# Kernel optimization log

Hardware: AMD Instinct MI355X
Metric: run time of the kernel (lower is better)

Reference implementation:

```python
import jax, jax.numpy as jnp
import numpy as np

B, S, H = 2, 2048, 2048
NH, G = 16, 4
HD = H // NH          # 128
REP = NH // G         # 4 query heads per KV group
KV = G * HD           # 512


def setup_inputs() -> dict:
    key = jax.random.key(0)
    ks = jax.random.split(key, 10)
    s = 0.02
    X = jax.random.normal(ks[0], (B, S, H), dtype=jnp.float32)
    Wq = jax.random.normal(ks[1], (H, H), dtype=jnp.float32) * s
    bq = jnp.zeros((H,), dtype=jnp.float32)
    Wk = jax.random.normal(ks[2], (H, KV), dtype=jnp.float32) * s
    bk = jnp.zeros((KV,), dtype=jnp.float32)
    Wv = jax.random.normal(ks[3], (H, KV), dtype=jnp.float32) * s
    bv = jnp.zeros((KV,), dtype=jnp.float32)
    Wo = jax.random.normal(ks[4], (H, H), dtype=jnp.float32) * s
    bo = jnp.zeros((H,), dtype=jnp.float32)
    # causal mask: 1 where attention is disallowed (strict upper triangle)
    casual_mask = jnp.triu(jnp.ones((S, S), dtype=jnp.float32), k=1)[None, None]
    return {"X": X, "Wq": Wq, "bq": bq, "Wk": Wk, "bk": bk,
            "Wv": Wv, "bv": bv, "Wo": Wo, "bo": bo,
            "casual_mask": casual_mask}


def reference(X, Wq, bq, Wk, bk, Wv, bv, Wo, bo, casual_mask):
    # projections
    q = X @ Wq + bq                          # [B,S,H]
    k = X @ Wk + bk                          # [B,S,G*HD]
    v = X @ Wv + bv                          # [B,S,G*HD]
    # split heads; q grouped as (group, rep) to match torch expand ordering
    q = q.reshape(B, S, NH, HD).transpose(0, 2, 1, 3)       # [B,NH,S,HD]
    q = q.reshape(B, G, REP, S, HD)                          # [B,G,REP,S,HD]
    k = k.reshape(B, S, G, HD).transpose(0, 2, 1, 3)         # [B,G,S,HD]
    v = v.reshape(B, S, G, HD).transpose(0, 2, 1, 3)         # [B,G,S,HD]
    scale = 1.0 / jnp.sqrt(jnp.float32(HD))
    scores = jnp.einsum('bgrqd,bgkd->bgrqk', q, k) * scale   # [B,G,REP,S,S]
    scores = scores + casual_mask * (-1e9)
    probs = jax.nn.softmax(scores, axis=-1)
    out = jnp.einsum('bgrqk,bgkd->bgrqd', probs, v)          # [B,G,REP,S,HD]
    out = out.reshape(B, NH, S, HD).transpose(0, 2, 1, 3).reshape(B, S, H)
    return out @ Wo + bo
```

## Files before the change

kernel.cpp:

```cpp
#include <hip/hip_runtime.h>

#define B_   2
#define S_   2048
#define H_   2048
#define NH_  16
#define G_   4
#define HD_  128
#define KV_  512
#define HQKV 3072

typedef __attribute__((ext_vector_type(8))) short bf16x8;
typedef __attribute__((ext_vector_type(4))) float f32x4;

__device__ __forceinline__ unsigned short f2bf(float f) {
    unsigned u = __float_as_uint(f);
    u += 0x7fff + ((u >> 16) & 1);
    return (unsigned short)(u >> 16);
}
__device__ __forceinline__ float bf2f(unsigned short s) {
    return __uint_as_float(((unsigned)s) << 16);
}

#define GLDS16(gsrc, ldst)                                                            \
    __builtin_amdgcn_global_load_lds(                                                 \
        (const __attribute__((address_space(1))) void*)(gsrc),                        \
        (__attribute__((address_space(3))) void*)(ldst), 16, 0, 0)

__global__ void k_cvt_bf16(const float* __restrict__ in, unsigned short* __restrict__ out, int n4) {
    int i = blockIdx.x * blockDim.x + threadIdx.x;
    if (i >= n4) return;
    float4 v = ((const float4*)in)[i];
    ushort4 o;
    o.x = f2bf(v.x); o.y = f2bf(v.y); o.z = f2bf(v.z); o.w = f2bf(v.w);
    ((ushort4*)out)[i] = o;
}

__global__ void k_transpose_cvt(const float* __restrict__ in, unsigned short* __restrict__ out,
                                int R, int C) {
    __shared__ float t[32][33];
    int c0 = blockIdx.x * 32, r0 = blockIdx.y * 32;
    int tx = threadIdx.x, ty = threadIdx.y;
#pragma unroll
    for (int i = 0; i < 4; ++i)
        t[ty + i*8][tx] = in[(size_t)(r0 + ty + i*8) * C + c0 + tx];
    __syncthreads();
#pragma unroll
    for (int i = 0; i < 4; ++i)
        out[(size_t)(c0 + ty + i*8) * R + r0 + tx] = f2bf(t[tx][ty + i*8]);
}

__global__ void k_concat_bias(const float* __restrict__ bq, const float* __restrict__ bk,
                              const float* __restrict__ bv, float* __restrict__ out) {
    int i = blockIdx.x * 256 + threadIdx.x;
    if (i >= HQKV) return;
    out[i] = (i < H_) ? bq[i] : (i < H_ + KV_ ? bk[i - H_] : bv[i - H_ - KV_]);
}

__global__ void k_transpose_v(const unsigned short* __restrict__ in, unsigned short* __restrict__ out) {
    __shared__ unsigned short t[32][33];
    int b = blockIdx.z;
    int c0 = blockIdx.x * 32, s0 = blockIdx.y * 32;
    int tx = threadIdx.x, ty = threadIdx.y;
#pragma unroll
    for (int i = 0; i < 4; ++i)
        t[ty + i*8][tx] = in[((size_t)b * S_ + s0 + ty + i*8) * HQKV + (H_ + KV_) + c0 + tx];
    __syncthreads();
#pragma unroll
    for (int i = 0; i < 4; ++i)
        out[((size_t)b * KV_ + c0 + ty + i*8) * S_ + s0 + tx] = t[tx][ty + i*8];
}

template <bool BF16OUT>
__global__ __launch_bounds__(256) void k_gemm_bt(
    const unsigned short* __restrict__ A, const unsigned short* __restrict__ Bt,
    const float* __restrict__ bias, void* __restrict__ Cout, int M, int N, int K) {
    __shared__ __align__(16) unsigned short As[128 * 64];
    __shared__ __align__(16) unsigned short Bs[128 * 64];
    const int tid = threadIdx.x, lane = tid & 63, w = tid >> 6;
    const int l15 = lane & 15, l4 = lane >> 4;
    const int wr = w >> 1, wc = w & 1;
    const int m0 = blockIdx.x * 128, n0 = blockIdx.y * 128;
    f32x4 acc[4][4] = {};

    for (int kt = 0; kt < K; kt += 64) {
        __syncthreads();
#pragma unroll
        for (int i = 0; i < 4; ++i) {
            int p = (w * 4 + i) * 64 + lane;
            int row = p >> 3, c = (p & 7) ^ (row & 7);
            GLDS16(A + (size_t)(m0 + row) * K + kt + c * 8, As + (size_t)(w * 4 + i) * 512);
        }
#pragma unroll
        for (int i = 0; i < 4; ++i) {
            int p = (w * 4 + i) * 64 + lane;
            int row = p >> 3, c = (p & 7) ^ (row & 7);
            GLDS16(Bt + (size_t)(n0 + row) * K + kt + c * 8, Bs + (size_t)(w * 4 + i) * 512);
        }
        __syncthreads();
#pragma unroll
        for (int ks = 0; ks < 2; ++ks) {
            bf16x8 af[4], bfr[4];
#pragma unroll
            for (int m = 0; m < 4; ++m) {
                int row = wr * 64 + m * 16 + l15;
                int ch = (ks * 4 + l4) ^ (row & 7);
                af[m] = *(const bf16x8*)(As + row * 64 + ch * 8);
            }
#pragma unroll
            for (int n = 0; n < 4; ++n) {
                int row = wc * 64 + n * 16 + l15;
                int ch = (ks * 4 + l4) ^ (row & 7);
                bfr[n] = *(const bf16x8*)(Bs + row * 64 + ch * 8);
            }
#pragma unroll
            for (int m = 0; m < 4; ++m)
#pragma unroll
                for (int n = 0; n < 4; ++n)
                    acc[m][n] = __builtin_amdgcn_mfma_f32_16x16x32_bf16(af[m], bfr[n], acc[m][n], 0, 0, 0);
        }
    }
#pragma unroll
    for (int m = 0; m < 4; ++m) {
        int row = m0 + wr * 64 + m * 16 + l4 * 4;
#pragma unroll
        for (int n = 0; n < 4; ++n) {
            int col = n0 + wc * 64 + n * 16 + l15;
            float bv = bias[col];
#pragma unroll
            for (int r = 0; r < 4; ++r) {
                float v = acc[m][n][r] + bv;
                if (BF16OUT)
                    ((unsigned short*)Cout)[(size_t)(row + r) * N + col] = f2bf(v);
                else
                    ((float*)Cout)[(size_t)(row + r) * N + col] = v;
            }
        }
    }
}

__global__ __launch_bounds__(256) void k_flash(
    const unsigned short* __restrict__ QKV,
    const unsigned short* __restrict__ VT,
    unsigned short* __restrict__ Oa) {
    __shared__ __align__(16) unsigned short Ks[2][64 * 128];
    __shared__ __align__(16) unsigned short Vs[2][128 * 64];
    __shared__ __align__(16) unsigned short Ps[4][16][68];
    const int tid = threadIdx.x, lane = tid & 63, w = tid >> 6;
    const int l15 = lane & 15, l4 = lane >> 4;
    const int bid = blockIdx.x;
    const int xcd = bid & 7, idx = bid >> 3;
    const int bh = xcd * 4 + (idx & 3);
    const int pr = idx >> 2;
    const int b = bh >> 4, nh = bh & 15, g = nh >> 2;
    const float sc2 = 0.08838834764831843f * 1.4426950408889634f;

    const unsigned short* kgbase = QKV + (size_t)b * S_ * HQKV + H_ + g * HD_;
    const unsigned short* vgbase = VT + ((size_t)b * KV_ + g * HD_) * S_;

    for (int half = 0; half < 2; ++half) {
        const int qt = half ? (31 - pr) : pr;
        const int q0 = qt * 64;
        const int qbase = q0 + w * 16;

        bf16x8 qf[4];
#pragma unroll
        for (int kb = 0; kb < 4; ++kb) {
            bf16x8 raw = *(const bf16x8*)(QKV + (size_t)(b * S_ + qbase + l15) * HQKV +
                                          nh * HD_ + kb * 32 + l4 * 8);
            bf16x8 sq;
#pragma unroll
            for (int e = 0; e < 8; ++e)
                sq[e] = (short)f2bf(bf2f((unsigned short)raw[e]) * sc2);
            qf[kb] = sq;
        }

        f32x4 o[8] = {};
        float mrow[4], lrow[4];
#pragma unroll
        for (int r = 0; r < 4; ++r) { mrow[r] = -1e30f; lrow[r] = 0.f; }

        auto issue = [&](int kt, int cb) {
            const int kv0 = kt * 64;
#pragma unroll
            for (int i = 0; i < 4; ++i) {
                int p = i * 256 + tid;
                int row = p >> 4, c = (p & 15) ^ (row & 15);
                GLDS16(kgbase + (size_t)(kv0 + row) * HQKV + c * 8,
                       &Ks[cb][(i * 256 + w * 64) * 8]);
            }
#pragma unroll
            for (int i = 0; i < 4; ++i) {
                int p = i * 256 + tid;
                int row = p >> 3, c = (p & 7) ^ (row & 7);
                GLDS16(vgbase + (size_t)row * S_ + kv0 + c * 8,
                       &Vs[cb][(i * 256 + w * 64) * 8]);
            }
        };

        auto compute = [&](int cb, int kt) {
            const int kv0 = kt * 64;
            f32x4 s[4] = {};
#pragma unroll
            for (int kb = 0; kb < 4; ++kb) {
                bf16x8 kf[4];
#pragma unroll
                for (int n = 0; n < 4; ++n) {
                    int row = n * 16 + l15;
                    int sl = (kb * 4 + l4) ^ (row & 15);
                    kf[n] = *(const bf16x8*)(&Ks[cb][(row * 16 + sl) * 8]);
                }
#pragma unroll
                for (int n = 0; n < 4; ++n)
                    s[n] = __builtin_amdgcn_mfma_f32_16x16x32_bf16(qf[kb], kf[n], s[n], 0, 0, 0);
            }
            if (kv0 + 63 > qbase) {
#pragma unroll
                for (int n = 0; n < 4; ++n)
#pragma unroll
                    for (int r = 0; r < 4; ++r) {
                        int kcol = kv0 + n * 16 + l15;
                        int qrow = qbase + l4 * 4 + r;
                        if (kcol > qrow) s[n][r] = -1e30f;
                    }
            }
            float vm[4];
#pragma unroll
            for (int r = 0; r < 4; ++r) {
                float v = fmaxf(fmaxf(s[0][r], s[1][r]), fmaxf(s[2][r], s[3][r]));
                v = fmaxf(v, __shfl_xor(v, 1));
                v = fmaxf(v, __shfl_xor(v, 2));
                v = fmaxf(v, __shfl_xor(v, 4));
                v = fmaxf(v, __shfl_xor(v, 8));
                vm[r] = v;
            }
            int needs = 0;
#pragma unroll
            for (int r = 0; r < 4; ++r) needs |= (vm[r] > mrow[r] + 8.0f) ? 1 : 0;
            if (__any(needs)) {
                float sf[4];
#pragma unroll
                for (int r = 0; r < 4; ++r) {
                    float mn = fmaxf(mrow[r], vm[r]);
                    sf[r] = exp2f(mrow[r] - mn);
                    mrow[r] = mn;
                    lrow[r] *= sf[r];
                }
#pragma unroll
                for (int nc = 0; nc < 8; ++nc) {
                    f32x4 t = o[nc];
                    t[0] *= sf[0]; t[1] *= sf[1]; t[2] *= sf[2]; t[3] *= sf[3];
                    o[nc] = t;
                }
            }
            float rs[4] = {0.f, 0.f, 0.f, 0.f};
#pragma unroll
            for (int n = 0; n < 4; ++n)
#pragma unroll
                for (int r = 0; r < 4; ++r) {
                    float p = exp2f(s[n][r] - mrow[r]);
                    s[n][r] = p;
                    rs[r] += p;
                }
#pragma unroll
            for (int r = 0; r < 4; ++r) {
                float t = rs[r];
                t += __shfl_xor(t, 1); t += __shfl_xor(t, 2);
                t += __shfl_xor(t, 4); t += __shfl_xor(t, 8);
                lrow[r] += t;
            }
#pragma unroll
            for (int n = 0; n < 4; ++n)
#pragma unroll
                for (int r = 0; r < 4; ++r)
                    Ps[w][l4 * 4 + r][n * 16 + l15] = f2bf(s[n][r]);
#pragma unroll
            for (int kb = 0; kb < 2; ++kb) {
                bf16x8 pf = *(const bf16x8*)(&Ps[w][l15][kb * 32 + l4 * 8]);
#pragma unroll
                for (int nc = 0; nc < 8; ++nc) {
                    int row = nc * 16 + l15;
                    int sl = (kb * 4 + l4) ^ (row & 7);
                    bf16x8 vf = *(const bf16x8*)(&Vs[cb][(row * 8 + sl) * 8]);
                    o[nc] = __builtin_amdgcn_mfma_f32_16x16x32_bf16(pf, vf, o[nc], 0, 0, 0);
                }
            }
        };

        const int nkt = qt + 1;
        __syncthreads();
        issue(0, 0);
        asm volatile("s_waitcnt vmcnt(0)" ::: "memory");
        __builtin_amdgcn_s_barrier();
        __builtin_amdgcn_sched_barrier(0);

        for (int kt = 0; kt < nkt; ++kt) {
            const int cb = kt & 1;
            if (kt + 1 < nkt) issue(kt + 1, cb ^ 1);
            compute(cb, kt);
            asm volatile("s_waitcnt vmcnt(0) lgkmcnt(0)" ::: "memory");
            __builtin_amdgcn_s_barrier();
            __builtin_amdgcn_sched_barrier(0);
        }

#pragma unroll
        for (int r = 0; r < 4; ++r) {
            float inv = 1.0f / lrow[r];
            int qrow = qbase + l4 * 4 + r;
            size_t base = (size_t)(b * S_ + qrow) * H_ + nh * HD_;
#pragma unroll
            for (int nc = 0; nc < 8; ++nc)
                Oa[base + nc * 16 + l15] = f2bf(o[nc][r] * inv);
        }
    }
}

extern "C" void kernel_launch(void* const* d_in, const int* in_sizes, int n_in,
                              void* d_out, int out_size, void* d_ws, size_t ws_size,
                              hipStream_t stream) {
    const float* X  = (const float*)d_in[0];
    const float* Wq = (const float*)d_in[1];
    const float* bq = (const float*)d_in[2];
    const float* Wk = (const float*)d_in[3];
    const float* bk = (const float*)d_in[4];
    const float* Wv = (const float*)d_in[5];
    const float* bv = (const float*)d_in[6];
    const float* Wo = (const float*)d_in[7];
    const float* bo = (const float*)d_in[8];
    float* out = (float*)d_out;

    if (ws_size < 67200000) return;
    char* ws = (char*)d_ws;
    unsigned short* Xb   = (unsigned short*)(ws);
    unsigned short* WqkvT= (unsigned short*)(ws + 16777216);
    unsigned short* WoT  = (unsigned short*)(ws + 29360128);
    unsigned short* QKV  = (unsigned short*)(ws + 37748736);
    unsigned short* VbT  = (unsigned short*)(ws + 62914560);
    float*          bqkv = (float*)(ws + 67108864);
    unsigned short* AOb  = Xb;

    k_cvt_bf16<<<(B_ * S_ * H_ / 4 + 255) / 256, 256, 0, stream>>>(X, Xb, B_ * S_ * H_ / 4);
    k_transpose_cvt<<<dim3(H_ / 32, H_ / 32), dim3(32, 8), 0, stream>>>(Wq, WqkvT, H_, H_);
    k_transpose_cvt<<<dim3(KV_ / 32, H_ / 32), dim3(32, 8), 0, stream>>>(Wk, WqkvT + (size_t)H_ * H_, H_, KV_);
    k_transpose_cvt<<<dim3(KV_ / 32, H_ / 32), dim3(32, 8), 0, stream>>>(Wv, WqkvT + (size_t)(H_ + KV_) * H_, H_, KV_);
    k_transpose_cvt<<<dim3(H_ / 32, H_ / 32), dim3(32, 8), 0, stream>>>(Wo, WoT, H_, H_);
    k_concat_bias<<<(HQKV + 255) / 256, 256, 0, stream>>>(bq, bk, bv, bqkv);

    k_gemm_bt<true><<<dim3(32, 24), 256, 0, stream>>>(Xb, WqkvT, bqkv, QKV, 4096, HQKV, 2048);

    k_transpose_v<<<dim3(KV_ / 32, S_ / 32, B_), dim3(32, 8), 0, stream>>>(QKV, VbT);
    k_flash<<<dim3(512), 256, 0, stream>>>(QKV, VbT, AOb);

    k_gemm_bt<false><<<dim3(32, 16), 256, 0, stream>>>(AOb, WoT, bo, out, 4096, 2048, 2048);
}
```

Measured before the change: 240.3 us.

## Read K/V fragments directly from global memory in flash kernel, fold Q scale into GEMM

The flash-attention kernel drops its double-buffered LDS staging of K and V tiles and the per-tile barriers. Each wave now loads its MFMA K and V fragments straight from global memory, relying on L2/L1 caching because the four waves share the same tiles. Removing the LDS buffers lets the kernel declare a higher occupancy target (launch_bounds 256,4). The softmax scale on Q moves into the QKV GEMM epilogue so the flash kernel loads Q directly. The trade is that shared tiles are no longer reused through LDS, so each wave issues redundant global loads with uncoalesced strided rows, in exchange for no synchronization and more resident waves.

After: 425.4 us. 1.77x slower.

```diff
diff --git a/kernel.cpp b/kernel.cpp
--- a/kernel.cpp
+++ b/kernel.cpp
@@ -17,14 +17,13 @@
     u += 0x7fff + ((u >> 16) & 1);
     return (unsigned short)(u >> 16);
 }
-__device__ __forceinline__ float bf2f(unsigned short s) {
-    return __uint_as_float(((unsigned)s) << 16);
-}
 
 #define GLDS16(gsrc, ldst)                                                            \
     __builtin_amdgcn_global_load_lds(                                                 \
         (const __attribute__((address_space(1))) void*)(gsrc),                        \
         (__attribute__((address_space(3))) void*)(ldst), 16, 0, 0)
+
+#define SC2F (0.08838834764831843f * 1.4426950408889634f)
 
 __global__ void k_cvt_bf16(const float* __restrict__ in, unsigned short* __restrict__ out, int n4) {
     int i = blockIdx.x * blockDim.x + threadIdx.x;
@@ -70,7 +69,7 @@
         out[((size_t)b * KV_ + c0 + ty + i*8) * S_ + s0 + tx] = t[tx][ty + i*8];
 }
 
-template <bool BF16OUT>
+template <bool BF16OUT, bool QSCALE>
 __global__ __launch_bounds__(256) void k_gemm_bt(
     const unsigned short* __restrict__ A, const unsigned short* __restrict__ Bt,
     const float* __restrict__ bias, void* __restrict__ Cout, int M, int N, int K) {
@@ -129,6 +128,7 @@
 #pragma unroll
             for (int r = 0; r < 4; ++r) {
                 float v = acc[m][n][r] + bv;
+                if (QSCALE) { if (col < H_) v *= SC2F; }
                 if (BF16OUT)
                     ((unsigned short*)Cout)[(size_t)(row + r) * N + col] = f2bf(v);
                 else
@@ -138,12 +138,10 @@
     }
 }
 
-__global__ __launch_bounds__(256) void k_flash(
+__global__ __launch_bounds__(256, 4) void k_flash(
     const unsigned short* __restrict__ QKV,
     const unsigned short* __restrict__ VT,
     unsigned short* __restrict__ Oa) {
-    __shared__ __align__(16) unsigned short Ks[2][64 * 128];
-    __shared__ __align__(16) unsigned short Vs[2][128 * 64];
     __shared__ __align__(16) unsigned short Ps[4][16][68];
     const int tid = threadIdx.x, lane = tid & 63, w = tid >> 6;
     const int l15 = lane & 15, l4 = lane >> 4;
@@ -152,7 +150,6 @@
     const int bh = xcd * 4 + (idx & 3);
     const int pr = idx >> 2;
     const int b = bh >> 4, nh = bh & 15, g = nh >> 2;
-    const float sc2 = 0.08838834764831843f * 1.4426950408889634f;
 
     const unsigned short* kgbase = QKV + (size_t)b * S_ * HQKV + H_ + g * HD_;
     const unsigned short* vgbase = VT + ((size_t)b * KV_ + g * HD_) * S_;
@@ -164,51 +161,28 @@
 
         bf16x8 qf[4];
 #pragma unroll
-        for (int kb = 0; kb < 4; ++kb) {
-            bf16x8 raw = *(const bf16x8*)(QKV + (size_t)(b * S_ + qbase + l15) * HQKV +
-                                          nh * HD_ + kb * 32 + l4 * 8);
-            bf16x8 sq;
-#pragma unroll
-            for (int e = 0; e < 8; ++e)
-                sq[e] = (short)f2bf(bf2f((unsigned short)raw[e]) * sc2);
-            qf[kb] = sq;
-        }
+        for (int kb = 0; kb < 4; ++kb)
+            qf[kb] = *(const bf16x8*)(QKV + (size_t)(b * S_ + qbase + l15) * HQKV +
+                                      nh * HD_ + kb * 32 + l4 * 8);
 
         f32x4 o[8] = {};
         float mrow[4], lrow[4];
 #pragma unroll
         for (int r = 0; r < 4; ++r) { mrow[r] = -1e30f; lrow[r] = 0.f; }
 
-        auto issue = [&](int kt, int cb) {
+        const int nkt = qt + 1;
+        for (int kt = 0; kt < nkt; ++kt) {
             const int kv0 = kt * 64;
-#pragma unroll
-            for (int i = 0; i < 4; ++i) {
-                int p = i * 256 + tid;
-                int row = p >> 4, c = (p & 15) ^ (row & 15);
-                GLDS16(kgbase + (size_t)(kv0 + row) * HQKV + c * 8,
-                       &Ks[cb][(i * 256 + w * 64) * 8]);
-            }
-#pragma unroll
-            for (int i = 0; i < 4; ++i) {
-                int p = i * 256 + tid;
-                int row = p >> 3, c = (p & 7) ^ (row & 7);
-                GLDS16(vgbase + (size_t)row * S_ + kv0 + c * 8,
-                       &Vs[cb][(i * 256 + w * 64) * 8]);
-            }
-        };
-
-        auto compute = [&](int cb, int kt) {
-            const int kv0 = kt * 64;
+            const unsigned short* kti = kgbase + (size_t)kv0 * HQKV;
+            const unsigned short* vti = vgbase + kv0;
+
             f32x4 s[4] = {};
 #pragma unroll
             for (int kb = 0; kb < 4; ++kb) {
                 bf16x8 kf[4];
 #pragma unroll
-                for (int n = 0; n < 4; ++n) {
-                    int row = n * 16 + l15;
-                    int sl = (kb * 4 + l4) ^ (row & 15);
-                    kf[n] = *(const bf16x8*)(&Ks[cb][(row * 16 + sl) * 8]);
-                }
+                for (int n = 0; n < 4; ++n)
+                    kf[n] = *(const bf16x8*)(kti + (size_t)(n * 16 + l15) * HQKV + kb * 32 + l4 * 8);
 #pragma unroll
                 for (int n = 0; n < 4; ++n)
                     s[n] = __builtin_amdgcn_mfma_f32_16x16x32_bf16(qf[kb], kf[n], s[n], 0, 0, 0);
@@ -278,30 +252,11 @@
                 bf16x8 pf = *(const bf16x8*)(&Ps[w][l15][kb * 32 + l4 * 8]);
 #pragma unroll
                 for (int nc = 0; nc < 8; ++nc) {
-                    int row = nc * 16 + l15;
-                    int sl = (kb * 4 + l4) ^ (row & 7);
-                    bf16x8 vf = *(const bf16x8*)(&Vs[cb][(row * 8 + sl) * 8]);
+                    bf16x8 vf = *(const bf16x8*)(vti + (size_t)(nc * 16 + l15) * S_ + kb * 32 + l4 * 8);
                     o[nc] = __builtin_amdgcn_mfma_f32_16x16x32_bf16(pf, vf, o[nc], 0, 0, 0);
                 }
             }
-        };
-
-        const int nkt = qt + 1;
-        __syncthreads();
-        issue(0, 0);
-        asm volatile("s_waitcnt vmcnt(0)" ::: "memory");
-        __builtin_amdgcn_s_barrier();
-        __builtin_amdgcn_sched_barrier(0);
-
-        for (int kt = 0; kt < nkt; ++kt) {
-            const int cb = kt & 1;
-            if (kt + 1 < nkt) issue(kt + 1, cb ^ 1);
-            compute(cb, kt);
-            asm volatile("s_waitcnt vmcnt(0) lgkmcnt(0)" ::: "memory");
-            __builtin_amdgcn_s_barrier();
-            __builtin_amdgcn_sched_barrier(0);
-        }
-
+        }
 #pragma unroll
         for (int r = 0; r < 4; ++r) {
             float inv = 1.0f / lrow[r];
@@ -345,10 +300,10 @@
     k_transpose_cvt<<<dim3(H_ / 32, H_ / 32), dim3(32, 8), 0, stream>>>(Wo, WoT, H_, H_);
     k_concat_bias<<<(HQKV + 255) / 256, 256, 0, stream>>>(bq, bk, bv, bqkv);
 
-    k_gemm_bt<true><<<dim3(32, 24), 256, 0, stream>>>(Xb, WqkvT, bqkv, QKV, 4096, HQKV, 2048);
+    k_gemm_bt<true, true><<<dim3(32, 24), 256, 0, stream>>>(Xb, WqkvT, bqkv, QKV, 4096, HQKV, 2048);
 
     k_transpose_v<<<dim3(KV_ / 32, S_ / 32, B_), dim3(32, 8), 0, stream>>>(QKV, VbT);
     k_flash<<<dim3(512), 256, 0, stream>>>(QKV, VbT, AOb);
 
-    k_gemm_bt<false><<<dim3(32, 16), 256, 0, stream>>>(AOb, WoT, bo, out, 4096, 2048, 2048);
-}
+    k_gemm_bt<false, false><<<dim3(32, 16), 256, 0, stream>>>(AOb, WoT, bo, out, 4096, 2048, 2048);
+}
```

## Split long causal query tiles across two blocks and merge with a combine kernel

Applied to the files above, without the earlier changes.

The flash kernel stops pairing short and long query tiles in one block. It now launches 1536 blocks: tiles 0-15 are done whole, and tiles 16-31 are split into KV ranges [0,16) and [16,qt]. Each split writes an unnormalized partial with its m/l statistics, and a new combine kernel merges them. It also folds the Q softmax scale into the QKV GEMM epilogue, single-buffers K with a mid-iteration reload, shrinks the P staging buffer, and sets launch_bounds occupancy 3. The aim is more parallelism and better load balance, at the cost of an extra kernel, partial-output traffic, and bf16 rounding of unnormalized partials.

Result: slower. 250.8 us (+4.4%).

```diff
diff --git a/kernel.cpp b/kernel.cpp
--- a/kernel.cpp
+++ b/kernel.cpp
@@ -26,6 +26,8 @@
         (const __attribute__((address_space(1))) void*)(gsrc),                        \
         (__attribute__((address_space(3))) void*)(ldst), 16, 0, 0)
 
+#define SC2F (0.08838834764831843f * 1.4426950408889634f)
+
 __global__ void k_cvt_bf16(const float* __restrict__ in, unsigned short* __restrict__ out, int n4) {
     int i = blockIdx.x * blockDim.x + threadIdx.x;
     if (i >= n4) return;
@@ -70,7 +72,7 @@
         out[((size_t)b * KV_ + c0 + ty + i*8) * S_ + s0 + tx] = t[tx][ty + i*8];
 }
 
-template <bool BF16OUT>
+template <bool BF16OUT, bool QSCALE>
 __global__ __launch_bounds__(256) void k_gemm_bt(
     const unsigned short* __restrict__ A, const unsigned short* __restrict__ Bt,
     const float* __restrict__ bias, void* __restrict__ Cout, int M, int N, int K) {
@@ -129,6 +131,7 @@
 #pragma unroll
             for (int r = 0; r < 4; ++r) {
                 float v = acc[m][n][r] + bv;
+                if (QSCALE) { if (col < H_) v *= SC2F; }
                 if (BF16OUT)
                     ((unsigned short*)Cout)[(size_t)(row + r) * N + col] = f2bf(v);
                 else
@@ -138,170 +141,170 @@
     }
 }
 
-__global__ __launch_bounds__(256) void k_flash(
+__global__ __launch_bounds__(256, 3) void k_flash(
     const unsigned short* __restrict__ QKV,
     const unsigned short* __restrict__ VT,
-    unsigned short* __restrict__ Oa) {
-    __shared__ __align__(16) unsigned short Ks[2][64 * 128];
+    unsigned short* __restrict__ Oa,
+    unsigned short* __restrict__ part1,
+    float* __restrict__ mlbuf) {
+    __shared__ __align__(16) unsigned short Ks[64 * 128];
     __shared__ __align__(16) unsigned short Vs[2][128 * 64];
-    __shared__ __align__(16) unsigned short Ps[4][16][68];
+    __shared__ __align__(16) unsigned short Ps[4][16][40];
     const int tid = threadIdx.x, lane = tid & 63, w = tid >> 6;
     const int l15 = lane & 15, l4 = lane >> 4;
     const int bid = blockIdx.x;
     const int xcd = bid & 7, idx = bid >> 3;
     const int bh = xcd * 4 + (idx & 3);
-    const int pr = idx >> 2;
+    const int jidx = idx >> 2;
     const int b = bh >> 4, nh = bh & 15, g = nh >> 2;
-    const float sc2 = 0.08838834764831843f * 1.4426950408889634f;
+
+    int qt, t0, t1, mode;
+    if (jidx < 16) { qt = 16 + jidx; t0 = 0; t1 = 16; mode = 1; }
+    else {
+        int k = jidx - 16, j = k >> 1;
+        if ((k & 1) == 0) { qt = 31 - j; t0 = 16; t1 = qt + 1; mode = 2; }
+        else              { qt = 15 - j; t0 = 0;  t1 = qt + 1; mode = 0; }
+    }
+    const int qbase = qt * 64 + w * 16;
 
     const unsigned short* kgbase = QKV + (size_t)b * S_ * HQKV + H_ + g * HD_;
     const unsigned short* vgbase = VT + ((size_t)b * KV_ + g * HD_) * S_;
 
-    for (int half = 0; half < 2; ++half) {
-        const int qt = half ? (31 - pr) : pr;
-        const int q0 = qt * 64;
-        const int qbase = q0 + w * 16;
-
-        bf16x8 qf[4];
-#pragma unroll
-        for (int kb = 0; kb < 4; ++kb) {
-            bf16x8 raw = *(const bf16x8*)(QKV + (size_t)(b * S_ + qbase + l15) * HQKV +
-                                          nh * HD_ + kb * 32 + l4 * 8);
-            bf16x8 sq;
-#pragma unroll
-            for (int e = 0; e < 8; ++e)
-                sq[e] = (short)f2bf(bf2f((unsigned short)raw[e]) * sc2);
-            qf[kb] = sq;
-        }
-
-        f32x4 o[8] = {};
-        float mrow[4], lrow[4];
-#pragma unroll
-        for (int r = 0; r < 4; ++r) { mrow[r] = -1e30f; lrow[r] = 0.f; }
-
-        auto issue = [&](int kt, int cb) {
-            const int kv0 = kt * 64;
-#pragma unroll
-            for (int i = 0; i < 4; ++i) {
-                int p = i * 256 + tid;
-                int row = p >> 4, c = (p & 15) ^ (row & 15);
-                GLDS16(kgbase + (size_t)(kv0 + row) * HQKV + c * 8,
-                       &Ks[cb][(i * 256 + w * 64) * 8]);
-            }
-#pragma unroll
-            for (int i = 0; i < 4; ++i) {
-                int p = i * 256 + tid;
-                int row = p >> 3, c = (p & 7) ^ (row & 7);
-                GLDS16(vgbase + (size_t)row * S_ + kv0 + c * 8,
-                       &Vs[cb][(i * 256 + w * 64) * 8]);
-            }
-        };
-
-        auto compute = [&](int cb, int kt) {
-            const int kv0 = kt * 64;
-            f32x4 s[4] = {};
-#pragma unroll
-            for (int kb = 0; kb < 4; ++kb) {
-                bf16x8 kf[4];
-#pragma unroll
-                for (int n = 0; n < 4; ++n) {
-                    int row = n * 16 + l15;
-                    int sl = (kb * 4 + l4) ^ (row & 15);
-                    kf[n] = *(const bf16x8*)(&Ks[cb][(row * 16 + sl) * 8]);
-                }
-#pragma unroll
-                for (int n = 0; n < 4; ++n)
-                    s[n] = __builtin_amdgcn_mfma_f32_16x16x32_bf16(qf[kb], kf[n], s[n], 0, 0, 0);
-            }
-            if (kv0 + 63 > qbase) {
-#pragma unroll
-                for (int n = 0; n < 4; ++n)
-#pragma unroll
-                    for (int r = 0; r < 4; ++r) {
-                        int kcol = kv0 + n * 16 + l15;
-                        int qrow = qbase + l4 * 4 + r;
-                        if (kcol > qrow) s[n][r] = -1e30f;
-                    }
-            }
-            float vm[4];
-#pragma unroll
-            for (int r = 0; r < 4; ++r) {
-                float v = fmaxf(fmaxf(s[0][r], s[1][r]), fmaxf(s[2][r], s[3][r]));
-                v = fmaxf(v, __shfl_xor(v, 1));
-                v = fmaxf(v, __shfl_xor(v, 2));
-                v = fmaxf(v, __shfl_xor(v, 4));
-                v = fmaxf(v, __shfl_xor(v, 8));
-                vm[r] = v;
-            }
-            int needs = 0;
-#pragma unroll
-            for (int r = 0; r < 4; ++r) needs |= (vm[r] > mrow[r] + 8.0f) ? 1 : 0;
-            if (__any(needs)) {
-                float sf[4];
-#pragma unroll
-                for (int r = 0; r < 4; ++r) {
-                    float mn = fmaxf(mrow[r], vm[r]);
-                    sf[r] = exp2f(mrow[r] - mn);
-                    mrow[r] = mn;
-                    lrow[r] *= sf[r];
-                }
-#pragma unroll
-                for (int nc = 0; nc < 8; ++nc) {
-                    f32x4 t = o[nc];
-                    t[0] *= sf[0]; t[1] *= sf[1]; t[2] *= sf[2]; t[3] *= sf[3];
-                    o[nc] = t;
-                }
-            }
-            float rs[4] = {0.f, 0.f, 0.f, 0.f};
-#pragma unroll
-            for (int n = 0; n < 4; ++n)
-#pragma unroll
-                for (int r = 0; r < 4; ++r) {
-                    float p = exp2f(s[n][r] - mrow[r]);
-                    s[n][r] = p;
-                    rs[r] += p;
-                }
-#pragma unroll
-            for (int r = 0; r < 4; ++r) {
-                float t = rs[r];
-                t += __shfl_xor(t, 1); t += __shfl_xor(t, 2);
-                t += __shfl_xor(t, 4); t += __shfl_xor(t, 8);
-                lrow[r] += t;
-            }
-#pragma unroll
-            for (int n = 0; n < 4; ++n)
-#pragma unroll
-                for (int r = 0; r < 4; ++r)
-                    Ps[w][l4 * 4 + r][n * 16 + l15] = f2bf(s[n][r]);
-#pragma unroll
-            for (int kb = 0; kb < 2; ++kb) {
-                bf16x8 pf = *(const bf16x8*)(&Ps[w][l15][kb * 32 + l4 * 8]);
-#pragma unroll
-                for (int nc = 0; nc < 8; ++nc) {
-                    int row = nc * 16 + l15;
-                    int sl = (kb * 4 + l4) ^ (row & 7);
-                    bf16x8 vf = *(const bf16x8*)(&Vs[cb][(row * 8 + sl) * 8]);
-                    o[nc] = __builtin_amdgcn_mfma_f32_16x16x32_bf16(pf, vf, o[nc], 0, 0, 0);
-                }
-            }
-        };
-
-        const int nkt = qt + 1;
-        __syncthreads();
-        issue(0, 0);
+    auto issueK = [&](int kt) {
+        const int kv0 = kt * 64;
+#pragma unroll
+        for (int i = 0; i < 4; ++i) {
+            int p = i * 256 + tid;
+            int row = p >> 4, c = (p & 15) ^ (row & 15);
+            GLDS16(kgbase + (size_t)(kv0 + row) * HQKV + c * 8, &Ks[(i * 256 + w * 64) * 8]);
+        }
+    };
+    auto issueV = [&](int kt) {
+        const int kv0 = kt * 64;
+        const int cb = kt & 1;
+#pragma unroll
+        for (int i = 0; i < 4; ++i) {
+            int p = i * 256 + tid;
+            int row = p >> 3, c = (p & 7) ^ (row & 7);
+            GLDS16(vgbase + (size_t)row * S_ + kv0 + c * 8, &Vs[cb][(i * 256 + w * 64) * 8]);
+        }
+    };
+
+    bf16x8 qf[4];
+#pragma unroll
+    for (int kb = 0; kb < 4; ++kb)
+        qf[kb] = *(const bf16x8*)(QKV + (size_t)(b * S_ + qbase + l15) * HQKV +
+                                  nh * HD_ + kb * 32 + l4 * 8);
+
+    f32x4 o[8] = {};
+    float mrow[4], lrow[4];
+#pragma unroll
+    for (int r = 0; r < 4; ++r) { mrow[r] = -1e30f; lrow[r] = 0.f; }
+
+    issueK(t0);
+    issueV(t0);
+
+    for (int kt = t0; kt < t1; ++kt) {
+        const int kv0 = kt * 64;
+        const int cb = kt & 1;
         asm volatile("s_waitcnt vmcnt(0)" ::: "memory");
         __builtin_amdgcn_s_barrier();
         __builtin_amdgcn_sched_barrier(0);
-
-        for (int kt = 0; kt < nkt; ++kt) {
-            const int cb = kt & 1;
-            if (kt + 1 < nkt) issue(kt + 1, cb ^ 1);
-            compute(cb, kt);
-            asm volatile("s_waitcnt vmcnt(0) lgkmcnt(0)" ::: "memory");
-            __builtin_amdgcn_s_barrier();
-            __builtin_amdgcn_sched_barrier(0);
-        }
-
+        if (kt + 1 < t1) issueV(kt + 1);
+
+        f32x4 s[4] = {};
+#pragma unroll
+        for (int kb = 0; kb < 4; ++kb) {
+            bf16x8 kf[4];
+#pragma unroll
+            for (int n = 0; n < 4; ++n) {
+                int row = n * 16 + l15;
+                int sl = (kb * 4 + l4) ^ (row & 15);
+                kf[n] = *(const bf16x8*)(&Ks[(row * 16 + sl) * 8]);
+            }
+#pragma unroll
+            for (int n = 0; n < 4; ++n)
+                s[n] = __builtin_amdgcn_mfma_f32_16x16x32_bf16(qf[kb], kf[n], s[n], 0, 0, 0);
+        }
+        if (kv0 + 63 > qbase) {
+#pragma unroll
+            for (int n = 0; n < 4; ++n)
+#pragma unroll
+                for (int r = 0; r < 4; ++r) {
+                    int kcol = kv0 + n * 16 + l15;
+                    int qrow = qbase + l4 * 4 + r;
+                    if (kcol > qrow) s[n][r] = -1e30f;
+                }
+        }
+        float vm[4];
+#pragma unroll
+        for (int r = 0; r < 4; ++r) {
+            float v = fmaxf(fmaxf(s[0][r], s[1][r]), fmaxf(s[2][r], s[3][r]));
+            v = fmaxf(v, __shfl_xor(v, 1));
+            v = fmaxf(v, __shfl_xor(v, 2));
+            v = fmaxf(v, __shfl_xor(v, 4));
+            v = fmaxf(v, __shfl_xor(v, 8));
+            vm[r] = v;
+        }
+        int needs = 0;
+#pragma unroll
+        for (int r = 0; r < 4; ++r) needs |= (vm[r] > mrow[r] + 8.0f) ? 1 : 0;
+        if (__any(needs)) {
+            float sf[4];
+#pragma unroll
+            for (int r = 0; r < 4; ++r) {
+                float mn = fmaxf(mrow[r], vm[r]);
+                sf[r] = exp2f(mrow[r] - mn);
+                mrow[r] = mn;
+                lrow[r] *= sf[r];
+            }
+#pragma unroll
+            for (int nc = 0; nc < 8; ++nc) {
+                f32x4 t = o[nc];
+                t[0] *= sf[0]; t[1] *= sf[1]; t[2] *= sf[2]; t[3] *= sf[3];
+                o[nc] = t;
+            }
+        }
+        float rs[4] = {0.f, 0.f, 0.f, 0.f};
+#pragma unroll
+        for (int n = 0; n < 4; ++n)
+#pragma unroll
+            for (int r = 0; r < 4; ++r) {
+                float p = exp2f(s[n][r] - mrow[r]);
+                s[n][r] = p;
+                rs[r] += p;
+            }
+#pragma unroll
+        for (int r = 0; r < 4; ++r) {
+            float t = rs[r];
+            t += __shfl_xor(t, 1); t += __shfl_xor(t, 2);
+            t += __shfl_xor(t, 4); t += __shfl_xor(t, 8);
+            lrow[r] += t;
+        }
+
+        __builtin_amdgcn_s_barrier();
+        __builtin_amdgcn_sched_barrier(0);
+        if (kt + 1 < t1) issueK(kt + 1);
+
+#pragma unroll
+        for (int h = 0; h < 2; ++h) {
+#pragma unroll
+            for (int n = 0; n < 2; ++n)
+#pragma unroll
+                for (int r = 0; r < 4; ++r)
+                    Ps[w][l4 * 4 + r][n * 16 + l15] = f2bf(s[2 * h + n][r]);
+            bf16x8 pf = *(const bf16x8*)(&Ps[w][l15][l4 * 8]);
+#pragma unroll
+            for (int nc = 0; nc < 8; ++nc) {
+                int row = nc * 16 + l15;
+                int sl = (h * 4 + l4) ^ (row & 7);
+                bf16x8 vf = *(const bf16x8*)(&Vs[cb][(row * 8 + sl) * 8]);
+                o[nc] = __builtin_amdgcn_mfma_f32_16x16x32_bf16(pf, vf, o[nc], 0, 0, 0);
+            }
+        }
+    }
+
+    if (mode == 0) {
 #pragma unroll
         for (int r = 0; r < 4; ++r) {
             float inv = 1.0f / lrow[r];
@@ -311,6 +314,67 @@
             for (int nc = 0; nc < 8; ++nc)
                 Oa[base + nc * 16 + l15] = f2bf(o[nc][r] * inv);
         }
+    } else {
+        const int base = bh * 16 + (qt - 16);
+        const int c = (mode == 1) ? 0 : 1;
+        float* mlrec = mlbuf + (size_t)(base * 2 + c) * 64 * 2;
+        if (l15 == 0) {
+#pragma unroll
+            for (int r = 0; r < 4; ++r) {
+                int row = w * 16 + l4 * 4 + r;
+                mlrec[row * 2 + 0] = mrow[r];
+                mlrec[row * 2 + 1] = lrow[r];
+            }
+        }
+        if (mode == 1) {
+#pragma unroll
+            for (int r = 0; r < 4; ++r) {
+                int qrow = qbase + l4 * 4 + r;
+                size_t ob = (size_t)(b * S_ + qrow) * H_ + nh * HD_;
+#pragma unroll
+                for (int nc = 0; nc < 8; ++nc)
+                    Oa[ob + nc * 16 + l15] = f2bf(o[nc][r]);
+            }
+        } else {
+#pragma unroll
+            for (int r = 0; r < 4; ++r) {
+                size_t pb = ((size_t)base * 64 + w * 16 + l4 * 4 + r) * 128;
+#pragma unroll
+                for (int nc = 0; nc < 8; ++nc)
+                    part1[pb + nc * 16 + l15] = f2bf(o[nc][r]);
+            }
+        }
+    }
+}
+
+__global__ __launch_bounds__(256) void k_combine(
+    const float* __restrict__ mlbuf, const unsigned short* __restrict__ part1,
+    unsigned short* __restrict__ Oa) {
+    int rec = blockIdx.x;
+    int bh = rec >> 4, qt = 16 + (rec & 15);
+    int b = bh >> 4, nh = bh & 15;
+    int row = threadIdx.x >> 2;
+    int dseg = (threadIdx.x & 3) * 32;
+    const float* ml0 = mlbuf + (size_t)(rec * 2 + 0) * 128;
+    const float* ml1 = mlbuf + (size_t)(rec * 2 + 1) * 128;
+    float m0 = ml0[row * 2], l0 = ml0[row * 2 + 1];
+    float m1 = ml1[row * 2], l1 = ml1[row * 2 + 1];
+    float M = fmaxf(m0, m1);
+    float a0 = exp2f(m0 - M), a1 = exp2f(m1 - M);
+    float L = a0 * l0 + a1 * l1;
+    float s0 = a0 / L, s1 = a1 / L;
+    size_t ob = ((size_t)(b * S_) + qt * 64 + row) * H_ + nh * HD_ + dseg;
+    const unsigned short* p1 = part1 + ((size_t)rec * 64 + row) * 128 + dseg;
+#pragma unroll
+    for (int i = 0; i < 4; ++i) {
+        bf16x8 v0 = *(const bf16x8*)(Oa + ob + i * 8);
+        bf16x8 v1 = *(const bf16x8*)(p1 + i * 8);
+        bf16x8 oo;
+#pragma unroll
+        for (int e = 0; e < 8; ++e)
+            oo[e] = (short)f2bf(bf2f((unsigned short)v0[e]) * s0 +
+                                bf2f((unsigned short)v1[e]) * s1);
+        *(bf16x8*)(Oa + ob + i * 8) = oo;
     }
 }
 
@@ -328,15 +392,17 @@
     const float* bo = (const float*)d_in[8];
     float* out = (float*)d_out;
 
-    if (ws_size < 67200000) return;
+    if (ws_size < 80000000) return;
     char* ws = (char*)d_ws;
-    unsigned short* Xb   = (unsigned short*)(ws);
-    unsigned short* WqkvT= (unsigned short*)(ws + 16777216);
-    unsigned short* WoT  = (unsigned short*)(ws + 29360128);
-    unsigned short* QKV  = (unsigned short*)(ws + 37748736);
-    unsigned short* VbT  = (unsigned short*)(ws + 62914560);
-    float*          bqkv = (float*)(ws + 67108864);
-    unsigned short* AOb  = Xb;
+    unsigned short* Xb    = (unsigned short*)(ws);
+    unsigned short* WqkvT = (unsigned short*)(ws + 16777216);
+    unsigned short* WoT   = (unsigned short*)(ws + 29360128);
+    unsigned short* QKV   = (unsigned short*)(ws + 37748736);
+    unsigned short* VbT   = (unsigned short*)(ws + 62914560);
+    unsigned short* part1 = (unsigned short*)(ws + 67108864);
+    float*          mlbuf = (float*)(ws + 75497472);
+    float*          bqkv  = (float*)(ws + 76021760);
+    unsigned short* AOb   = Xb;
 
     k_cvt_bf16<<<(B_ * S_ * H_ / 4 + 255) / 256, 256, 0, stream>>>(X, Xb, B_ * S_ * H_ / 4);
     k_transpose_cvt<<<dim3(H_ / 32, H_ / 32), dim3(32, 8), 0, stream>>>(Wq, WqkvT, H_, H_);
@@ -345,10 +411,11 @@
     k_transpose_cvt<<<dim3(H_ / 32, H_ / 32), dim3(32, 8), 0, stream>>>(Wo, WoT, H_, H_);
     k_concat_bias<<<(HQKV + 255) / 256, 256, 0, stream>>>(bq, bk, bv, bqkv);
 
-    k_gemm_bt<true><<<dim3(32, 24), 256, 0, stream>>>(Xb, WqkvT, bqkv, QKV, 4096, HQKV, 2048);
+    k_gemm_bt<true, true><<<dim3(32, 24), 256, 0, stream>>>(Xb, WqkvT, bqkv, QKV, 4096, HQKV, 2048);
 
     k_transpose_v<<<dim3(KV_ / 32, S_ / 32, B_), dim3(32, 8), 0, stream>>>(QKV, VbT);
-    k_flash<<<dim3(512), 256, 0, stream>>>(QKV, VbT, AOb);
-
-    k_gemm_bt<false><<<dim3(32, 16), 256, 0, stream>>>(AOb, WoT, bo, out, 4096, 2048, 2048);
-}
+    k_flash<<<dim3(1536), 256, 0, stream>>>(QKV, VbT, AOb, part1, mlbuf);
+    k_combine<<<dim3(512), 256, 0, stream>>>(mlbuf, part1, AOb);
+
+    k_gemm_bt<false, false><<<dim3(32, 16), 256, 0, stream>>>(AOb, WoT, bo, out, 4096, 2048, 2048);
+}
```
